# Optimization experiments

Measured on AMD Instinct MI355X. Metric: run time of the kernel, lower is better.

Reference implementation:

```python
import jax, jax.numpy as jnp
import numpy as np

EPS = 1e-7


def setup_inputs() -> dict:
    key = jax.random.key(0)
    k1, k2, k3, k4 = jax.random.split(key, 4)
    N, M = 8192, 8192
    inputs = jax.random.normal(k1, (N, 2), dtype=jnp.float32)
    outputs = jax.random.normal(k2, (N,), dtype=jnp.float32)
    x = jax.random.normal(k3, (M, 2), dtype=jnp.float32)
    # positive per-query bandwidths in [0.5, 1.5)
    bandwidth = 0.5 + jax.random.uniform(k4, (M,), dtype=jnp.float32)
    return {"x": x, "inputs": inputs, "outputs": outputs, "bandwidth": bandwidth}


def reference(x, inputs, outputs, bandwidth):
    # Squared pairwise distances (cdist followed by .pow(2) in the original):
    # d2[n, m] = ||inputs[n] - x[m]||^2, computed via the expansion to avoid
    # materializing an (N, M, 2) intermediate.
    a2 = jnp.sum(inputs * inputs, axis=1)  # (N,)
    b2 = jnp.sum(x * x, axis=1)            # (M,)
    d2 = a2[:, None] + b2[None, :] - 2.0 * (inputs @ x.T)  # (N, M)
    d2 = jnp.maximum(d2, 0.0)

    bw = bandwidth[None, :]  # (1, M), per-query bandwidth
    weights = jnp.exp(-d2 / (2.0 * bw * bw))  # (N, M)
    # Normalization over dim 0 (over the N reference points)
    weights = weights / (jnp.sum(weights, axis=0, keepdims=True) + EPS)
    # weights.T @ outputs -> (M,), Nadaraya-Watson weighted sum
    weighted = weights.T @ outputs  # (M,)
    return weighted
```

## Files before the change

kernel.cpp:

```cpp
#include <hip/hip_runtime.h>

#define EPS 1e-7f
#define LOG2E 1.44269504088896340736f

typedef float f32x2 __attribute__((ext_vector_type(2)));
typedef float f32x4 __attribute__((ext_vector_type(4)));

constexpr int BLOCK = 1024;
constexpr int JJ    = 8;
constexpr int JR    = 4;
constexpr int JB    = JJ * JR;
constexpr int SS    = BLOCK / JJ;
constexpr int SEGN  = 8192;
constexpr int PTS   = SEGN / SS;
constexpr int ROW   = PTS + 4;

__global__ __launch_bounds__(BLOCK, 4) void nw_block(
    const float2* __restrict__ x,
    const float2* __restrict__ inputs,
    const float*  __restrict__ outputs,
    const float*  __restrict__ bw,
    float*        __restrict__ out,
    int N, int M)
{
    __shared__ float sA[4][SS][ROW];

    const int tid = threadIdx.x;
    const int jj  = tid & (JJ - 1);
    const int ss  = tid >> 3;
    const int j0  = blockIdx.x * JB;

    f32x2 c0p[JR], c1p[JR], c2p[JR], c3p[JR];
    #pragma unroll
    for (int r = 0; r < JR; ++r) {
        const int j = j0 + jj + r * JJ;
        float k = 0.f, v1 = 0.f, v2 = 0.f, v3 = 0.f;
        if (j < M) {
            float2 xj = x[j];
            float  b  = bw[j];
            k  = -LOG2E / (2.0f * b * b);
            v1 = -2.0f * k * xj.x;
            v2 = -2.0f * k * xj.y;
            v3 = k * fmaf(xj.x, xj.x, xj.y * xj.y);
        }
        c0p[r] = {k, k}; c1p[r] = {v1, v1}; c2p[r] = {v2, v2}; c3p[r] = {v3, v3};
    }

    f32x2 nump[JR], denp[JR];
    #pragma unroll
    for (int r = 0; r < JR; ++r) { nump[r] = {0.f, 0.f}; denp[r] = {0.f, 0.f}; }

    for (int s0 = 0; s0 < N; s0 += SEGN) {
        #pragma unroll
        for (int k = 0; k < SEGN / BLOCK; ++k) {
            const int i  = tid + k * BLOCK;
            const int gi = s0 + i;
            float2 p = make_float2(0.f, 0.f);
            float  o = 0.f, s = 3.0e38f;
            if (gi < N) { p = inputs[gi]; o = outputs[gi]; s = fmaf(p.x, p.x, p.y * p.y); }
            const int r = i >> 6;
            const int c = i & (PTS - 1);
            sA[0][r][c] = p.x;
            sA[1][r][c] = p.y;
            sA[2][r][c] = s;
            sA[3][r][c] = o;
        }
        __syncthreads();

        #pragma unroll 4
        for (int g = 0; g < PTS / 4; ++g) {
            f32x4 xq = *(const f32x4*)&sA[0][ss][4 * g];
            f32x4 yq = *(const f32x4*)&sA[1][ss][4 * g];
            f32x4 sq = *(const f32x4*)&sA[2][ss][4 * g];
            f32x4 oq = *(const f32x4*)&sA[3][ss][4 * g];
            f32x2 x0 = {xq.x, xq.y}, x1 = {xq.z, xq.w};
            f32x2 y0 = {yq.x, yq.y}, y1 = {yq.z, yq.w};
            f32x2 s0p = {sq.x, sq.y}, s1p = {sq.z, sq.w};
            f32x2 o0 = {oq.x, oq.y}, o1 = {oq.z, oq.w};
            #pragma unroll
            for (int r = 0; r < JR; ++r) {
                f32x2 ta = __builtin_elementwise_fma(c2p[r], y0, c3p[r]);
                ta = __builtin_elementwise_fma(c1p[r], x0, ta);
                ta = __builtin_elementwise_fma(c0p[r], s0p, ta);
                f32x2 tb = __builtin_elementwise_fma(c2p[r], y1, c3p[r]);
                tb = __builtin_elementwise_fma(c1p[r], x1, tb);
                tb = __builtin_elementwise_fma(c0p[r], s1p, tb);
                f32x2 wa, wb;
                wa.x = __builtin_amdgcn_exp2f(ta.x);
                wa.y = __builtin_amdgcn_exp2f(ta.y);
                wb.x = __builtin_amdgcn_exp2f(tb.x);
                wb.y = __builtin_amdgcn_exp2f(tb.y);
                nump[r] = __builtin_elementwise_fma(wa, o0, nump[r]);
                nump[r] = __builtin_elementwise_fma(wb, o1, nump[r]);
                denp[r] += wa + wb;
            }
        }
        __syncthreads();
    }

    float2 (*red)[JB] = (float2 (*)[JB]) & sA[0][0][0];
    #pragma unroll
    for (int r = 0; r < JR; ++r)
        red[ss][jj + r * JJ] = make_float2(nump[r].x + nump[r].y,
                                           denp[r].x + denp[r].y);
    __syncthreads();
    if (tid < 16 * JB) {
        const int s2   = tid >> 5;
        const int slot = tid & (JB - 1);
        float n = 0.f, d = 0.f;
        #pragma unroll
        for (int k = 0; k < SS / 16; ++k) {
            n += red[s2 + 16 * k][slot].x;
            d += red[s2 + 16 * k][slot].y;
        }
        red[s2][slot] = make_float2(n, d);
    }
    __syncthreads();
    if (tid < JB) {
        float n = 0.f, d = 0.f;
        #pragma unroll
        for (int s = 0; s < 16; ++s) {
            n += red[s][tid].x;
            d += red[s][tid].y;
        }
        const int j = j0 + tid;
        if (j < M) out[j] = n / (d + EPS);
    }
}

extern "C" void kernel_launch(void* const* d_in, const int* in_sizes, int n_in,
                              void* d_out, int out_size, void* d_ws, size_t ws_size,
                              hipStream_t stream) {
    const float2* x       = (const float2*)d_in[0];
    const float2* inputs  = (const float2*)d_in[1];
    const float*  outputs = (const float*) d_in[2];
    const float*  bwv     = (const float*) d_in[3];
    const int N = in_sizes[2];
    const int M = in_sizes[3];
    float*        out     = (float*)d_out;

    dim3 grid((M + JB - 1) / JB);
    nw_block<<<grid, BLOCK, 0, stream>>>(x, inputs, outputs, bwv, out, N, M);
}
```

Baseline: 72.94 us.

## Halve queries per block, stream inputs in register-prefetched chunks, Horner-form exponent

Query columns per block drop from 32 to 16, so the grid doubles and blocks spread more evenly across CUs. The launch bound goes from 4 to 2. Reference points are now staged through shared memory in 1024-point chunks, and the next chunk is prefetched into registers while the current one is computed. The exponent is rewritten in nested form, which removes the precomputed squared-norm array but adds one FMA per pair. The cost is a barrier every 1024 points and slightly more ALU work per exp.

```diff
diff --git a/kernel.cpp b/kernel.cpp
--- a/kernel.cpp
+++ b/kernel.cpp
@@ -7,15 +7,16 @@
 typedef float f32x4 __attribute__((ext_vector_type(4)));
 
 constexpr int BLOCK = 1024;
-constexpr int JJ    = 8;
+constexpr int JJ    = 4;
 constexpr int JR    = 4;
 constexpr int JB    = JJ * JR;
 constexpr int SS    = BLOCK / JJ;
-constexpr int SEGN  = 8192;
-constexpr int PTS   = SEGN / SS;
-constexpr int ROW   = PTS + 4;
+constexpr int CHUNK = 1024;
+constexpr int PTS   = CHUNK / SS;
+constexpr int ROW   = 12;
+constexpr int ASZ   = SS * ROW;
 
-__global__ __launch_bounds__(BLOCK, 4) void nw_block(
+__global__ __launch_bounds__(BLOCK, 2) void nw_block(
     const float2* __restrict__ x,
     const float2* __restrict__ inputs,
     const float*  __restrict__ outputs,
@@ -23,11 +24,14 @@
     float*        __restrict__ out,
     int N, int M)
 {
-    __shared__ float sA[4][SS][ROW];
+    __shared__ __align__(16) float smem[3 * ASZ];
+    float* sX = smem;
+    float* sY = smem + ASZ;
+    float* sO = smem + 2 * ASZ;
 
     const int tid = threadIdx.x;
     const int jj  = tid & (JJ - 1);
-    const int ss  = tid >> 3;
+    const int ss  = tid >> 2;
     const int j0  = blockIdx.x * JB;
 
     f32x2 c0p[JR], c1p[JR], c2p[JR], c3p[JR];
@@ -50,41 +54,42 @@
     #pragma unroll
     for (int r = 0; r < JR; ++r) { nump[r] = {0.f, 0.f}; denp[r] = {0.f, 0.f}; }
 
-    for (int s0 = 0; s0 < N; s0 += SEGN) {
-        #pragma unroll
-        for (int k = 0; k < SEGN / BLOCK; ++k) {
-            const int i  = tid + k * BLOCK;
-            const int gi = s0 + i;
-            float2 p = make_float2(0.f, 0.f);
-            float  o = 0.f, s = 3.0e38f;
-            if (gi < N) { p = inputs[gi]; o = outputs[gi]; s = fmaf(p.x, p.x, p.y * p.y); }
-            const int r = i >> 6;
-            const int c = i & (PTS - 1);
-            sA[0][r][c] = p.x;
-            sA[1][r][c] = p.y;
-            sA[2][r][c] = s;
-            sA[3][r][c] = o;
+    float2 pin = make_float2(0.f, 0.f);
+    float  po  = 0.f;
+    if (tid < N) { pin = inputs[tid]; po = outputs[tid]; }
+
+    for (int base = 0; base < N; base += CHUNK) {
+        {
+            const bool v = (base + tid) < N;
+            sX[ss * ROW + jj] = v ? pin.x : 1.0e19f;
+            sY[ss * ROW + jj] = v ? pin.y : 0.f;
+            sO[ss * ROW + jj] = v ? po    : 0.f;
         }
         __syncthreads();
 
-        #pragma unroll 4
-        for (int g = 0; g < PTS / 4; ++g) {
-            f32x4 xq = *(const f32x4*)&sA[0][ss][4 * g];
-            f32x4 yq = *(const f32x4*)&sA[1][ss][4 * g];
-            f32x4 sq = *(const f32x4*)&sA[2][ss][4 * g];
-            f32x4 oq = *(const f32x4*)&sA[3][ss][4 * g];
-            f32x2 x0 = {xq.x, xq.y}, x1 = {xq.z, xq.w};
-            f32x2 y0 = {yq.x, yq.y}, y1 = {yq.z, yq.w};
-            f32x2 s0p = {sq.x, sq.y}, s1p = {sq.z, sq.w};
-            f32x2 o0 = {oq.x, oq.y}, o1 = {oq.z, oq.w};
+        {
+            const int nb = base + CHUNK;
+            const int gi = nb + tid;
+            if (nb < N && gi < N) { pin = inputs[gi]; po = outputs[gi]; }
+        }
+
+        {
+            const f32x4 xq = *(const f32x4*)&sX[ss * ROW];
+            const f32x4 yq = *(const f32x4*)&sY[ss * ROW];
+            const f32x4 oq = *(const f32x4*)&sO[ss * ROW];
+            const f32x2 x0 = {xq.x, xq.y}, x1 = {xq.z, xq.w};
+            const f32x2 y0 = {yq.x, yq.y}, y1 = {yq.z, yq.w};
+            const f32x2 o0 = {oq.x, oq.y}, o1 = {oq.z, oq.w};
             #pragma unroll
             for (int r = 0; r < JR; ++r) {
-                f32x2 ta = __builtin_elementwise_fma(c2p[r], y0, c3p[r]);
-                ta = __builtin_elementwise_fma(c1p[r], x0, ta);
-                ta = __builtin_elementwise_fma(c0p[r], s0p, ta);
-                f32x2 tb = __builtin_elementwise_fma(c2p[r], y1, c3p[r]);
-                tb = __builtin_elementwise_fma(c1p[r], x1, tb);
-                tb = __builtin_elementwise_fma(c0p[r], s1p, tb);
+                f32x2 Aa = __builtin_elementwise_fma(c0p[r], x0, c1p[r]);
+                f32x2 Ba = __builtin_elementwise_fma(c0p[r], y0, c2p[r]);
+                f32x2 ta = __builtin_elementwise_fma(Ba, y0, c3p[r]);
+                ta = __builtin_elementwise_fma(Aa, x0, ta);
+                f32x2 Ab = __builtin_elementwise_fma(c0p[r], x1, c1p[r]);
+                f32x2 Bb = __builtin_elementwise_fma(c0p[r], y1, c2p[r]);
+                f32x2 tb = __builtin_elementwise_fma(Bb, y1, c3p[r]);
+                tb = __builtin_elementwise_fma(Ab, x1, tb);
                 f32x2 wa, wb;
                 wa.x = __builtin_amdgcn_exp2f(ta.x);
                 wa.y = __builtin_amdgcn_exp2f(ta.y);
@@ -98,14 +103,14 @@
         __syncthreads();
     }
 
-    float2 (*red)[JB] = (float2 (*)[JB]) & sA[0][0][0];
+    float2 (*red)[JB] = (float2 (*)[JB])smem;
     #pragma unroll
     for (int r = 0; r < JR; ++r)
         red[ss][jj + r * JJ] = make_float2(nump[r].x + nump[r].y,
                                            denp[r].x + denp[r].y);
     __syncthreads();
     if (tid < 16 * JB) {
-        const int s2   = tid >> 5;
+        const int s2   = tid >> 4;
         const int slot = tid & (JB - 1);
         float n = 0.f, d = 0.f;
         #pragma unroll
```

Result: slower. 76.23 us (+4.5%).
